# Kernel optimization log

Measured on AMD Instinct MI355X. Metric: run time of the kernel, lower is better.

The kernel has to match this reference:

```python
import jax, jax.numpy as jnp
import numpy as np

B, N, C, H = 2, 2048, 512, 8
D = C // H
SCALE = D ** (-0.5)


def setup_inputs() -> dict:
    key = jax.random.key(0)
    k1, k2, k3 = jax.random.split(key, 3)
    x = jax.random.normal(k1, (B, N, C), dtype=jnp.float32)
    qkv_w = jax.random.normal(k2, (C, 3 * C), dtype=jnp.float32) * (C ** -0.5)
    proj_w = jax.random.normal(k3, (C, C), dtype=jnp.float32) * (C ** -0.5)
    proj_b = jnp.zeros((C,), dtype=jnp.float32)
    return {"x": x, "qkv_w": qkv_w, "proj_w": proj_w, "proj_b": proj_b}


def reference(x, qkv_w, proj_w, proj_b):
    # qkv projection (no bias) -> (B, N, 3, H, D) -> (3, B, H, N, D)
    qkv = jnp.einsum('bnc,cf->bnf', x, qkv_w)
    qkv = qkv.reshape(B, N, 3, H, D).transpose(2, 0, 3, 1, 4)
    q, k, v = qkv[0], qkv[1], qkv[2]
    q = q * SCALE
    attn = jnp.einsum('bhid,bhjd->bhij', q, k)          # (B, H, N, N)
    attn = jax.nn.softmax(attn, axis=-1)
    out = jnp.einsum('bhij,bhjd->bhid', attn, v)         # (B, H, N, D)
    # Faithful to source: reshape (B,H,N,D) -> (B,N,C) WITHOUT transposing
    out = out.reshape(B, N, C)
    out = jnp.einsum('bnc,cd->bnd', out, proj_w) + proj_b
    return out
```

## Files before the change

### kernel.cpp

```cpp
#include <hip/hip_runtime.h>
#include <math.h>

constexpr int Bb = 2;
constexpr int Nn = 2048;
constexpr int Cc = 512;
constexpr int Hh = 8;
constexpr int Dd = 64;

typedef short short8 __attribute__((ext_vector_type(8)));
typedef float floatx4 __attribute__((ext_vector_type(4)));
typedef float floatx16 __attribute__((ext_vector_type(16)));

__device__ inline short8 bcs8(uint4 u) { return __builtin_bit_cast(short8, u); }

__device__ inline floatx4 mfma16(short8 a, short8 b, floatx4 c) {
    return __builtin_amdgcn_mfma_f32_16x16x32_bf16(a, b, c, 0, 0, 0);
}
__device__ inline floatx16 mfma32(short8 a, short8 b, floatx16 c) {
    return __builtin_amdgcn_mfma_f32_32x32x16_bf16(a, b, c, 0, 0, 0);
}

#if __has_builtin(__builtin_amdgcn_exp2f)
#define EXP2(x) __builtin_amdgcn_exp2f(x)
#else
#define EXP2(x) __expf((x) * 0.69314718056f)
#endif

__device__ inline unsigned pk_trunc(float a, float b) {
    return __builtin_amdgcn_perm(__float_as_uint(b), __float_as_uint(a), 0x07060302u);
}
__device__ inline unsigned pk_rne(float a, float b) {
    unsigned ua = __float_as_uint(a); ua += 0x7fffu + ((ua >> 16) & 1u);
    unsigned ub = __float_as_uint(b); ub += 0x7fffu + ((ub >> 16) & 1u);
    return __builtin_amdgcn_perm(ub, ua, 0x07060302u);
}
__device__ inline unsigned short rne1(float a) {
    unsigned u = __float_as_uint(a); u += 0x7fffu + ((u >> 16) & 1u);
    return (unsigned short)(u >> 16);
}
__device__ inline float tr16(float a) {
    return __uint_as_float(__float_as_uint(a) & 0xffff0000u);
}
__device__ inline void split8(float4 A, float4 B, uint4& hi, uint4& lo) {
    hi = make_uint4(pk_trunc(A.x, A.y), pk_trunc(A.z, A.w),
                    pk_trunc(B.x, B.y), pk_trunc(B.z, B.w));
    lo = make_uint4(pk_trunc(A.x - tr16(A.x), A.y - tr16(A.y)),
                    pk_trunc(A.z - tr16(A.z), A.w - tr16(A.w)),
                    pk_trunc(B.x - tr16(B.x), B.y - tr16(B.y)),
                    pk_trunc(B.z - tr16(B.z), B.w - tr16(B.w)));
}


__global__ __launch_bounds__(256) void prep(const float* __restrict__ qkv_w,
                                            const float* __restrict__ proj_w,
                                            const float* __restrict__ x,
                                            unsigned short* __restrict__ wqfrag,
                                            unsigned short* __restrict__ wpfrag,
                                            unsigned short* __restrict__ xfrag)
{
    __shared__ float Tl[64][68];
    int bid = blockIdx.x;
    int t = threadIdx.x;
    if (bid >= 256) {
        int xb = bid - 256;
        int tok = xb * 16 + (t >> 4);
        int kc = t & 15;
        const float* px = x + (size_t)tok * 512 + kc * 32;
        uint4 h[4], l[4];
        #pragma unroll
        for (int o = 0; o < 4; ++o) {
            float4 fa = *(const float4*)(px + o * 8);
            float4 fb = *(const float4*)(px + o * 8 + 4);
            split8(fa, fb, h[o], l[o]);
        }
        int mt = tok >> 4, m = tok & 15;
        unsigned short* fb_ = xfrag + ((size_t)(mt * 16 + kc) * 2) * 512;
        #pragma unroll
        for (int o = 0; o < 4; ++o) {
            *(uint4*)(fb_ + (m + 16 * o) * 8) = h[o];
            *(uint4*)(fb_ + 512 + (m + 16 * o) * 8) = l[o];
        }
        return;
    }
    const float* src; unsigned short* dfrag; int W, f0, k0;
    if (bid < 192) { int kt = bid / 24, ft = bid % 24; W = 1536; src = qkv_w; dfrag = wqfrag; f0 = ft * 64; k0 = kt * 64; }
    else { int b2 = bid - 192; int kt = b2 / 8, ft = b2 % 8; W = 512; src = proj_w; dfrag = wpfrag; f0 = ft * 64; k0 = kt * 64; }
    {
        int kl = t >> 2, fc = (t & 3) * 16;
        const float* p = src + (size_t)(k0 + kl) * W + f0 + fc;
        #pragma unroll
        for (int i = 0; i < 4; ++i) {
            float4 v = *(const float4*)(p + i * 4);
            Tl[kl][fc + i * 4 + 0] = v.x; Tl[kl][fc + i * 4 + 1] = v.y;
            Tl[kl][fc + i * 4 + 2] = v.z; Tl[kl][fc + i * 4 + 3] = v.w;
        }
    }
    __syncthreads();
    {
        int fl = t >> 2, kc16 = (t & 3) * 16;
        float v[16];
        #pragma unroll
        for (int i = 0; i < 16; ++i) v[i] = Tl[kc16 + i][fl];
        unsigned hi[8], lo[8];
        #pragma unroll
        for (int i = 0; i < 8; ++i) {
            float a = v[2 * i], b = v[2 * i + 1];
            hi[i] = pk_trunc(a, b);
            lo[i] = pk_trunc(a - tr16(a), b - tr16(b));
        }
        int f = f0 + fl;
        int nt = f >> 4, nin = f & 15;
        int kc = (k0 + kc16) >> 5;
        int oct0 = (kc16 >> 3) & 3;
        unsigned short* fb_ = dfrag + ((size_t)(nt * 16 + kc) * 2) * 512;
        *(uint4*)(fb_ + (nin + 16 * oct0) * 8) = make_uint4(hi[0], hi[1], hi[2], hi[3]);
        *(uint4*)(fb_ + (nin + 16 * (oct0 + 1)) * 8) = make_uint4(hi[4], hi[5], hi[6], hi[7]);
        *(uint4*)(fb_ + 512 + (nin + 16 * oct0) * 8) = make_uint4(lo[0], lo[1], lo[2], lo[3]);
        *(uint4*)(fb_ + 512 + (nin + 16 * (oct0 + 1)) * 8) = make_uint4(lo[4], lo[5], lo[6], lo[7]);
    }
}

__global__ __launch_bounds__(256, 4) void gemm_qkv(const unsigned short* __restrict__ xfrag,
                                                   const unsigned short* __restrict__ wqfrag,
                                                   unsigned short* __restrict__ qd,
                                                   unsigned short* __restrict__ kfrag,
                                                   unsigned short* __restrict__ vfrag)
{
    const int tid = threadIdx.x, lane = tid & 63, w = tid >> 6;
    const int l15 = lane & 15, l4 = lane >> 4;
    const int row0 = blockIdx.y * 64, col0 = blockIdx.x * 128;
    const int mt0 = row0 >> 4;
    const int nt0 = (col0 >> 4) + w * 2;

    floatx4 acc[4][2];
    #pragma unroll
    for (int i = 0; i < 4; ++i)
        #pragma unroll
        for (int j = 0; j < 2; ++j)
            #pragma unroll
            for (int r = 0; r < 4; ++r) acc[i][j][r] = 0.f;

    const unsigned short* xb = xfrag + (size_t)lane * 8;
    const unsigned short* wb = wqfrag + (size_t)lane * 8;

    #pragma unroll
    for (int kc = 0; kc < 16; ++kc) {
        short8 bf[2][2];
        #pragma unroll
        for (int nt = 0; nt < 2; ++nt) {
            size_t fb_ = ((size_t)((nt0 + nt) * 16 + kc) * 2) * 512;
            bf[nt][0] = bcs8(*(const uint4*)(wb + fb_));
            bf[nt][1] = bcs8(*(const uint4*)(wb + fb_ + 512));
        }
        #pragma unroll
        for (int mt = 0; mt < 4; ++mt) {
            size_t fa_ = ((size_t)((mt0 + mt) * 16 + kc) * 2) * 512;
            short8 ah = bcs8(*(const uint4*)(xb + fa_));
            short8 al = bcs8(*(const uint4*)(xb + fa_ + 512));
            #pragma unroll
            for (int nt = 0; nt < 2; ++nt) {
                acc[mt][nt] = mfma16(ah, bf[nt][0], acc[mt][nt]);
                acc[mt][nt] = mfma16(ah, bf[nt][1], acc[mt][nt]);
                acc[mt][nt] = mfma16(al, bf[nt][0], acc[mt][nt]);
            }
        }
    }
    #pragma unroll
    for (int mt = 0; mt < 4; ++mt)
        #pragma unroll
        for (int nt = 0; nt < 2; ++nt) {
            int c = col0 + (w * 2 + nt) * 16 + l15;
            int which = c >> 9;
            int head = (c >> 6) & 7, d = c & 63;
            int tokb = row0 + mt * 16 + l4 * 4;
            int b = tokb >> 11, n = tokb & 2047;
            int bh = b * 8 + head;
            if (which == 0) {
                #pragma unroll
                for (int r = 0; r < 4; ++r)
                    qd[(size_t)(bh * 2048 + n + r) * 64 + d] = rne1(acc[mt][nt][r] * 0.18033688f);
            } else if (which == 1) {
                int s = d >> 4;
                size_t fb_ = ((size_t)(bh * 64 + (n >> 5)) * 4 + s) * 512 + (d & 7);
                int hl = ((d >> 3) & 1) * 32;
                #pragma unroll
                for (int r = 0; r < 4; ++r)
                    kfrag[fb_ + (size_t)(hl + ((n + r) & 31)) * 8] = rne1(acc[mt][nt][r]);
            } else {
                int j = n >> 4, mtv = d >> 5;
                uint2 pv;
                pv.x = pk_rne(acc[mt][nt][0], acc[mt][nt][1]);
                pv.y = pk_rne(acc[mt][nt][2], acc[mt][nt][3]);
                *(uint2*)&vfrag[((size_t)(bh * 128 + j) * 2 + mtv) * 512 +
                                (size_t)(((n >> 3) & 1) * 32 + (d & 31)) * 8 + (n & 7)] = pv;
            }
        }
}

__global__ __launch_bounds__(256, 4) void attn(const unsigned short* __restrict__ qd,
                                               const unsigned short* __restrict__ kfrag,
                                               const unsigned short* __restrict__ vfrag,
                                               unsigned short* __restrict__ Ofrag)
{
    __shared__ float Ms[2048];
    __shared__ float Ls[64];
    __shared__ float Ts[2176];

    int bid = blockIdx.x;
    int xcd = bid & 7; int rr = bid >> 3;
    int qt = rr & 63; int bhi = rr >> 6;
    int bh = (bhi << 3) | xcd;
    int tid = threadIdx.x, lane = tid & 63, kg = tid >> 6;
    int l31 = lane & 31, h = lane >> 5;

    short8 qf[4];
    #pragma unroll
    for (int s = 0; s < 4; ++s)
        qf[s] = bcs8(*(const uint4*)(qd + ((size_t)bh * 2048 + qt * 32 + l31) * 64 + s * 16 + h * 8));

    const uint4 onesu = make_uint4(0x3F803F80u, 0x3F803F80u, 0x3F803F80u, 0x3F803F80u);
    const short8 onesf = bcs8(onesu);

    floatx16 OT[2], OTl;
    #pragma unroll
    for (int i = 0; i < 2; ++i)
        #pragma unroll
        for (int r = 0; r < 16; ++r) OT[i][r] = 0.f;
    #pragma unroll
    for (int r = 0; r < 16; ++r) OTl[r] = 0.f;

    const unsigned short* kb_ = kfrag + ((size_t)(bh * 64 + kg * 16) * 4) * 512 + lane * 8;
    const unsigned short* vb_ = vfrag + ((size_t)(bh * 128 + kg * 32) * 2) * 512 + lane * 8;

    #pragma unroll
    for (int c = 0; c < 16; ++c) {
        uint4 kfu[4];
        #pragma unroll
        for (int s = 0; s < 4; ++s)
            kfu[s] = *(const uint4*)(kb_ + ((size_t)c * 4 + s) * 512);
        uint4 vfu[2][2];
        #pragma unroll
        for (int kc = 0; kc < 2; ++kc)
            #pragma unroll
            for (int mtv = 0; mtv < 2; ++mtv)
                vfu[kc][mtv] = *(const uint4*)(vb_ + ((size_t)(c * 2 + kc) * 2 + mtv) * 512);

        floatx16 st;
        #pragma unroll
        for (int r = 0; r < 16; ++r) st[r] = 0.f;
        #pragma unroll
        for (int s = 0; s < 4; ++s) st = mfma32(bcs8(kfu[s]), qf[s], st);

        unsigned P2[8];
        #pragma unroll
        for (int s2 = 0; s2 < 8; ++s2)
            P2[s2] = pk_trunc(EXP2(st[2 * s2]), EXP2(st[2 * s2 + 1]));

        #pragma unroll
        for (int kc = 0; kc < 2; ++kc) {
            unsigned X0 = P2[4 * kc + 0], X1 = P2[4 * kc + 1];
            unsigned Y0 = P2[4 * kc + 2], Y1 = P2[4 * kc + 3];
            unsigned T0 = h ? X0 : Y0;
            unsigned T1 = h ? X1 : Y1;
            unsigned To0 = __shfl_xor(T0, 32, 64);
            unsigned To1 = __shfl_xor(T1, 32, 64);
            uint4 fu;
            fu.x = h ? To0 : X0;
            fu.y = h ? To1 : X1;
            fu.z = h ? Y0 : To0;
            fu.w = h ? Y1 : To1;
            short8 pf = bcs8(fu);
            OT[0] = mfma32(bcs8(vfu[kc][0]), pf, OT[0]);
            OT[1] = mfma32(bcs8(vfu[kc][1]), pf, OT[1]);
            OTl = mfma32(onesf, pf, OTl);
        }
    }

    if (kg == 3) {
        #pragma unroll
        for (int mtv = 0; mtv < 2; ++mtv)
            #pragma unroll
            for (int r = 0; r < 16; ++r) {
                int d = mtv * 32 + (r & 3) + 8 * (r >> 2) + 4 * h;
                Ms[d * 32 + l31] = OT[mtv][r];
            }
        Ls[h * 32 + l31] = OTl[0];
    }
    __syncthreads();
    if (kg == 2) {
        #pragma unroll
        for (int mtv = 0; mtv < 2; ++mtv)
            #pragma unroll
            for (int r = 0; r < 16; ++r) {
                int d = mtv * 32 + (r & 3) + 8 * (r >> 2) + 4 * h;
                Ms[d * 32 + l31] += OT[mtv][r];
            }
        Ls[h * 32 + l31] += OTl[0];
    }
    __syncthreads();
    if (kg == 1) {
        #pragma unroll
        for (int mtv = 0; mtv < 2; ++mtv)
            #pragma unroll
            for (int r = 0; r < 16; ++r) {
                int d = mtv * 32 + (r & 3) + 8 * (r >> 2) + 4 * h;
                Ms[d * 32 + l31] += OT[mtv][r];
            }
        Ls[h * 32 + l31] += OTl[0];
    }
    __syncthreads();
    if (kg == 0) {
        #pragma unroll
        for (int mtv = 0; mtv < 2; ++mtv)
            #pragma unroll
            for (int r = 0; r < 16; ++r) {
                int d = mtv * 32 + (r & 3) + 8 * (r >> 2) + 4 * h;
                OT[mtv][r] += Ms[d * 32 + l31];
            }
        float inv = 1.f / (Ls[h * 32 + l31] + OTl[0]);
        #pragma unroll
        for (int mtv = 0; mtv < 2; ++mtv)
            #pragma unroll
            for (int r = 0; r < 16; ++r) {
                int d = mtv * 32 + (r & 3) + 8 * (r >> 2) + 4 * h;
                Ts[l31 * 68 + d] = OT[mtv][r] * inv;
            }
    }
    __syncthreads();
    {
        int q = tid >> 3, dc = (tid & 7) * 8;
        float vv[8];
        #pragma unroll
        for (int i = 0; i < 8; ++i) vv[i] = Ts[q * 68 + dc + i];
        unsigned hi[4], lo[4];
        #pragma unroll
        for (int i = 0; i < 4; ++i) {
            float a = vv[2 * i], bb = vv[2 * i + 1];
            hi[i] = pk_trunc(a, bb);
            lo[i] = pk_trunc(a - tr16(a), bb - tr16(bb));
        }
        int ng = qt * 32 + q;
        int r = bh * 256 + (ng >> 3);
        int cc = (ng & 7) * 64 + dc;
        int mt = r >> 4, m = r & 15, kc = cc >> 5, oct = (cc >> 3) & 3;
        unsigned short* fb_ = Ofrag + ((size_t)(mt * 16 + kc) * 2) * 512 + (m + 16 * oct) * 8;
        *(uint4*)fb_ = make_uint4(hi[0], hi[1], hi[2], hi[3]);
        *(uint4*)(fb_ + 512) = make_uint4(lo[0], lo[1], lo[2], lo[3]);
    }
}

__global__ __launch_bounds__(256, 4) void gemm_proj(const unsigned short* __restrict__ Ofrag,
                                                    const unsigned short* __restrict__ wpfrag,
                                                    const float* __restrict__ bias,
                                                    float* __restrict__ out)
{
    const int tid = threadIdx.x, lane = tid & 63, w = tid >> 6;
    const int l15 = lane & 15, l4 = lane >> 4;
    const int row0 = blockIdx.y * 64, col0 = blockIdx.x * 64;
    const int wm = w >> 1, wn = w & 1;
    const int mt0 = (row0 >> 4) + wm * 2;
    const int nt0 = (col0 >> 4) + wn * 2;

    floatx4 acc[2][2];
    #pragma unroll
    for (int i = 0; i < 2; ++i)
        #pragma unroll
        for (int j = 0; j < 2; ++j)
            #pragma unroll
            for (int r = 0; r < 4; ++r) acc[i][j][r] = 0.f;

    const unsigned short* ab = Ofrag + (size_t)lane * 8;
    const unsigned short* wb = wpfrag + (size_t)lane * 8;

    #pragma unroll
    for (int kc = 0; kc < 16; ++kc) {
        short8 bf[2][2];
        #pragma unroll
        for (int nt = 0; nt < 2; ++nt) {
            size_t fb_ = ((size_t)((nt0 + nt) * 16 + kc) * 2) * 512;
            bf[nt][0] = bcs8(*(const uint4*)(wb + fb_));
            bf[nt][1] = bcs8(*(const uint4*)(wb + fb_ + 512));
        }
        #pragma unroll
        for (int mt = 0; mt < 2; ++mt) {
            size_t fa_ = ((size_t)((mt0 + mt) * 16 + kc) * 2) * 512;
            short8 ah = bcs8(*(const uint4*)(ab + fa_));
            short8 al = bcs8(*(const uint4*)(ab + fa_ + 512));
            #pragma unroll
            for (int nt = 0; nt < 2; ++nt) {
                acc[mt][nt] = mfma16(ah, bf[nt][0], acc[mt][nt]);
                acc[mt][nt] = mfma16(ah, bf[nt][1], acc[mt][nt]);
                acc[mt][nt] = mfma16(al, bf[nt][0], acc[mt][nt]);
            }
        }
    }
    #pragma unroll
    for (int mt = 0; mt < 2; ++mt)
        #pragma unroll
        for (int nt = 0; nt < 2; ++nt) {
            int c = col0 + wn * 32 + nt * 16 + l15;
            float bv = bias[c];
            #pragma unroll
            for (int r = 0; r < 4; ++r) {
                int tok = row0 + wm * 32 + mt * 16 + l4 * 4 + r;
                out[(size_t)tok * 512 + c] = acc[mt][nt][r] + bv;
            }
        }
}

extern "C" void kernel_launch(void* const* d_in, const int* in_sizes, int n_in,
                              void* d_out, int out_size, void* d_ws, size_t ws_size,
                              hipStream_t stream)
{
    const float* x      = (const float*)d_in[0];
    const float* qkv_w  = (const float*)d_in[1];
    const float* proj_w = (const float*)d_in[2];
    const float* proj_b = (const float*)d_in[3];
    float* out = (float*)d_out;

    char* ws = (char*)d_ws;
    unsigned short* xfrag  = (unsigned short*)ws;
    unsigned short* wqfrag = (unsigned short*)(ws + 8388608);
    unsigned short* wpfrag = (unsigned short*)(ws + 11534336);
    unsigned short* qd     = (unsigned short*)(ws + 12582912);
    unsigned short* kfrag  = (unsigned short*)(ws + 16777216);
    unsigned short* vfrag  = (unsigned short*)(ws + 20971520);
    unsigned short* Ofrag  = (unsigned short*)(ws + 25165824);

    prep<<<512, 256, 0, stream>>>(qkv_w, proj_w, x, wqfrag, wpfrag, xfrag);
    gemm_qkv<<<dim3(12, 64), 256, 0, stream>>>(xfrag, wqfrag, qd, kfrag, vfrag);
    attn<<<1024, 256, 0, stream>>>(qd, kfrag, vfrag, Ofrag);
    gemm_proj<<<dim3(8, 64), 256, 0, stream>>>(Ofrag, wpfrag, proj_b, out);
}
```

Measured before the change: 140.4 us.

## Process two query tiles per attention block to reuse K/V fragments

```diff
diff --git a/kernel.cpp b/kernel.cpp
--- a/kernel.cpp
+++ b/kernel.cpp
@@ -120,7 +120,7 @@
     }
 }
 
-__global__ __launch_bounds__(256, 4) void gemm_qkv(const unsigned short* __restrict__ xfrag,
+__global__ __launch_bounds__(256, 3) void gemm_qkv(const unsigned short* __restrict__ xfrag,
                                                    const unsigned short* __restrict__ wqfrag,
                                                    unsigned short* __restrict__ qd,
                                                    unsigned short* __restrict__ kfrag,
@@ -197,37 +197,42 @@
         }
 }
 
-__global__ __launch_bounds__(256, 4) void attn(const unsigned short* __restrict__ qd,
+__global__ __launch_bounds__(256, 2) void attn(const unsigned short* __restrict__ qd,
                                                const unsigned short* __restrict__ kfrag,
                                                const unsigned short* __restrict__ vfrag,
                                                unsigned short* __restrict__ Ofrag)
 {
-    __shared__ float Ms[2048];
-    __shared__ float Ls[64];
-    __shared__ float Ts[2176];
+    __shared__ float Ms[4096];
+    __shared__ float Ls[128];
+    __shared__ float Ts[64 * 68];
 
     int bid = blockIdx.x;
     int xcd = bid & 7; int rr = bid >> 3;
-    int qt = rr & 63; int bhi = rr >> 6;
+    int qt = rr & 31; int bhi = rr >> 5;
     int bh = (bhi << 3) | xcd;
     int tid = threadIdx.x, lane = tid & 63, kg = tid >> 6;
     int l31 = lane & 31, h = lane >> 5;
 
-    short8 qf[4];
-    #pragma unroll
-    for (int s = 0; s < 4; ++s)
-        qf[s] = bcs8(*(const uint4*)(qd + ((size_t)bh * 2048 + qt * 32 + l31) * 64 + s * 16 + h * 8));
+    short8 qf[2][4];
+    #pragma unroll
+    for (int qh = 0; qh < 2; ++qh)
+        #pragma unroll
+        for (int s = 0; s < 4; ++s)
+            qf[qh][s] = bcs8(*(const uint4*)(qd + ((size_t)bh * 2048 + qt * 64 + qh * 32 + l31) * 64 + s * 16 + h * 8));
 
     const uint4 onesu = make_uint4(0x3F803F80u, 0x3F803F80u, 0x3F803F80u, 0x3F803F80u);
     const short8 onesf = bcs8(onesu);
 
-    floatx16 OT[2], OTl;
-    #pragma unroll
-    for (int i = 0; i < 2; ++i)
-        #pragma unroll
-        for (int r = 0; r < 16; ++r) OT[i][r] = 0.f;
-    #pragma unroll
-    for (int r = 0; r < 16; ++r) OTl[r] = 0.f;
+    floatx16 OT[2][2], OTl[2];
+    #pragma unroll
+    for (int qh = 0; qh < 2; ++qh) {
+        #pragma unroll
+        for (int i = 0; i < 2; ++i)
+            #pragma unroll
+            for (int r = 0; r < 16; ++r) OT[qh][i][r] = 0.f;
+        #pragma unroll
+        for (int r = 0; r < 16; ++r) OTl[qh][r] = 0.f;
+    }
 
     const unsigned short* kb_ = kfrag + ((size_t)(bh * 64 + kg * 16) * 4) * 512 + lane * 8;
     const unsigned short* vb_ = vfrag + ((size_t)(bh * 128 + kg * 32) * 2) * 512 + lane * 8;
@@ -245,111 +250,130 @@
             for (int mtv = 0; mtv < 2; ++mtv)
                 vfu[kc][mtv] = *(const uint4*)(vb_ + ((size_t)(c * 2 + kc) * 2 + mtv) * 512);
 
-        floatx16 st;
-        #pragma unroll
-        for (int r = 0; r < 16; ++r) st[r] = 0.f;
-        #pragma unroll
-        for (int s = 0; s < 4; ++s) st = mfma32(bcs8(kfu[s]), qf[s], st);
-
-        unsigned P2[8];
-        #pragma unroll
-        for (int s2 = 0; s2 < 8; ++s2)
-            P2[s2] = pk_trunc(EXP2(st[2 * s2]), EXP2(st[2 * s2 + 1]));
-
-        #pragma unroll
-        for (int kc = 0; kc < 2; ++kc) {
-            unsigned X0 = P2[4 * kc + 0], X1 = P2[4 * kc + 1];
-            unsigned Y0 = P2[4 * kc + 2], Y1 = P2[4 * kc + 3];
-            unsigned T0 = h ? X0 : Y0;
-            unsigned T1 = h ? X1 : Y1;
-            unsigned To0 = __shfl_xor(T0, 32, 64);
-            unsigned To1 = __shfl_xor(T1, 32, 64);
-            uint4 fu;
-            fu.x = h ? To0 : X0;
-            fu.y = h ? To1 : X1;
-            fu.z = h ? Y0 : To0;
-            fu.w = h ? Y1 : To1;
-            short8 pf = bcs8(fu);
-            OT[0] = mfma32(bcs8(vfu[kc][0]), pf, OT[0]);
-            OT[1] = mfma32(bcs8(vfu[kc][1]), pf, OT[1]);
-            OTl = mfma32(onesf, pf, OTl);
+        #pragma unroll
+        for (int qh = 0; qh < 2; ++qh) {
+            floatx16 st;
+            #pragma unroll
+            for (int r = 0; r < 16; ++r) st[r] = 0.f;
+            #pragma unroll
+            for (int s = 0; s < 4; ++s) st = mfma32(bcs8(kfu[s]), qf[qh][s], st);
+
+            unsigned P2[8];
+            #pragma unroll
+            for (int s2 = 0; s2 < 8; ++s2)
+                P2[s2] = pk_trunc(EXP2(st[2 * s2]), EXP2(st[2 * s2 + 1]));
+
+            #pragma unroll
+            for (int kc = 0; kc < 2; ++kc) {
+                unsigned X0 = P2[4 * kc + 0], X1 = P2[4 * kc + 1];
+                unsigned Y0 = P2[4 * kc + 2], Y1 = P2[4 * kc + 3];
+                unsigned T0 = h ? X0 : Y0;
+                unsigned T1 = h ? X1 : Y1;
+                unsigned To0 = __shfl_xor(T0, 32, 64);
+                unsigned To1 = __shfl_xor(T1, 32, 64);
+                uint4 fu;
+                fu.x = h ? To0 : X0;
+                fu.y = h ? To1 : X1;
+                fu.z = h ? Y0 : To0;
+                fu.w = h ? Y1 : To1;
+                short8 pf = bcs8(fu);
+                OT[qh][0] = mfma32(bcs8(vfu[kc][0]), pf, OT[qh][0]);
+                OT[qh][1] = mfma32(bcs8(vfu[kc][1]), pf, OT[qh][1]);
+                OTl[qh] = mfma32(onesf, pf, OTl[qh]);
+            }
         }
     }
 
     if (kg == 3) {
         #pragma unroll
-        for (int mtv = 0; mtv < 2; ++mtv)
-            #pragma unroll
-            for (int r = 0; r < 16; ++r) {
-                int d = mtv * 32 + (r & 3) + 8 * (r >> 2) + 4 * h;
-                Ms[d * 32 + l31] = OT[mtv][r];
-            }
-        Ls[h * 32 + l31] = OTl[0];
+        for (int qh = 0; qh < 2; ++qh) {
+            #pragma unroll
+            for (int mtv = 0; mtv < 2; ++mtv)
+                #pragma unroll
+                for (int r = 0; r < 16; ++r) {
+                    int d = mtv * 32 + (r & 3) + 8 * (r >> 2) + 4 * h;
+                    Ms[d * 64 + qh * 32 + l31] = OT[qh][mtv][r];
+                }
+            Ls[h * 64 + qh * 32 + l31] = OTl[qh][0];
+        }
     }
     __syncthreads();
     if (kg == 2) {
         #pragma unroll
-        for (int mtv = 0; mtv < 2; ++mtv)
-            #pragma unroll
-            for (int r = 0; r < 16; ++r) {
-                int d = mtv * 32 + (r & 3) + 8 * (r >> 2) + 4 * h;
-                Ms[d * 32 + l31] += OT[mtv][r];
-            }
-        Ls[h * 32 + l31] += OTl[0];
+        for (int qh = 0; qh < 2; ++qh) {
+            #pragma unroll
+            for (int mtv = 0; mtv < 2; ++mtv)
+                #pragma unroll
+                for (int r = 0; r < 16; ++r) {
+                    int d = mtv * 32 + (r & 3) + 8 * (r >> 2) + 4 * h;
+                    Ms[d * 64 + qh * 32 + l31] += OT[qh][mtv][r];
+                }
+            Ls[h * 64 + qh * 32 + l31] += OTl[qh][0];
+        }
     }
     __syncthreads();
     if (kg == 1) {
         #pragma unroll
-        for (int mtv = 0; mtv < 2; ++mtv)
-            #pragma unroll
-            for (int r = 0; r < 16; ++r) {
-                int d = mtv * 32 + (r & 3) + 8 * (r >> 2) + 4 * h;
-                Ms[d * 32 + l31] += OT[mtv][r];
-            }
-        Ls[h * 32 + l31] += OTl[0];
+        for (int qh = 0; qh < 2; ++qh) {
+            #pragma unroll
+            for (int mtv = 0; mtv < 2; ++mtv)
+                #pragma unroll
+                for (int r = 0; r < 16; ++r) {
+                    int d = mtv * 32 + (r & 3) + 8 * (r >> 2) + 4 * h;
+                    Ms[d * 64 + qh * 32 + l31] += OT[qh][mtv][r];
+                }
+            Ls[h * 64 + qh * 32 + l31] += OTl[qh][0];
+        }
     }
     __syncthreads();
     if (kg == 0) {
         #pragma unroll
-        for (int mtv = 0; mtv < 2; ++mtv)
-            #pragma unroll
-            for (int r = 0; r < 16; ++r) {
-                int d = mtv * 32 + (r & 3) + 8 * (r >> 2) + 4 * h;
-                OT[mtv][r] += Ms[d * 32 + l31];
-            }
-        float inv = 1.f / (Ls[h * 32 + l31] + OTl[0]);
-        #pragma unroll
-        for (int mtv = 0; mtv < 2; ++mtv)
-            #pragma unroll
-            for (int r = 0; r < 16; ++r) {
-                int d = mtv * 32 + (r & 3) + 8 * (r >> 2) + 4 * h;
-                Ts[l31 * 68 + d] = OT[mtv][r] * inv;
-            }
+        for (int qh = 0; qh < 2; ++qh) {
+            #pragma unroll
+            for (int mtv = 0; mtv < 2; ++mtv)
+                #pragma unroll
+                for (int r = 0; r < 16; ++r) {
+                    int d = mtv * 32 + (r & 3) + 8 * (r >> 2) + 4 * h;
+                    OT[qh][mtv][r] += Ms[d * 64 + qh * 32 + l31];
+                }
+            float inv = 1.f / (Ls[h * 64 + qh * 32 + l31] + OTl[qh][0]);
+            #pragma unroll
+            for (int mtv = 0; mtv < 2; ++mtv)
+                #pragma unroll
+                for (int r = 0; r < 16; ++r) {
+                    int d = mtv * 32 + (r & 3) + 8 * (r >> 2) + 4 * h;
+                    Ts[(qh * 32 + l31) * 68 + d] = OT[qh][mtv][r] * inv;
+                }
+        }
     }
     __syncthreads();
     {
-        int q = tid >> 3, dc = (tid & 7) * 8;
-        float vv[8];
-        #pragma unroll
-        for (int i = 0; i < 8; ++i) vv[i] = Ts[q * 68 + dc + i];
-        unsigned hi[4], lo[4];
-        #pragma unroll
-        for (int i = 0; i < 4; ++i) {
+        int q = tid >> 2, dc = (tid & 3) * 16;
+        float vv[16];
+        #pragma unroll
+        for (int i = 0; i < 16; ++i) vv[i] = Ts[q * 68 + dc + i];
+        unsigned hi[8], lo[8];
+        #pragma unroll
+        for (int i = 0; i < 8; ++i) {
             float a = vv[2 * i], bb = vv[2 * i + 1];
             hi[i] = pk_trunc(a, bb);
             lo[i] = pk_trunc(a - tr16(a), bb - tr16(bb));
         }
-        int ng = qt * 32 + q;
+        int ng = qt * 64 + q;
         int r = bh * 256 + (ng >> 3);
-        int cc = (ng & 7) * 64 + dc;
-        int mt = r >> 4, m = r & 15, kc = cc >> 5, oct = (cc >> 3) & 3;
-        unsigned short* fb_ = Ofrag + ((size_t)(mt * 16 + kc) * 2) * 512 + (m + 16 * oct) * 8;
-        *(uint4*)fb_ = make_uint4(hi[0], hi[1], hi[2], hi[3]);
-        *(uint4*)(fb_ + 512) = make_uint4(lo[0], lo[1], lo[2], lo[3]);
-    }
-}
-
-__global__ __launch_bounds__(256, 4) void gemm_proj(const unsigned short* __restrict__ Ofrag,
+        int mt = r >> 4, m = r & 15;
+        #pragma unroll
+        for (int hh = 0; hh < 2; ++hh) {
+            int cc = (ng & 7) * 64 + dc + hh * 8;
+            int kc = cc >> 5, oct = (cc >> 3) & 3;
+            unsigned short* fb_ = Ofrag + ((size_t)(mt * 16 + kc) * 2) * 512 + (m + 16 * oct) * 8;
+            *(uint4*)fb_ = make_uint4(hi[4 * hh + 0], hi[4 * hh + 1], hi[4 * hh + 2], hi[4 * hh + 3]);
+            *(uint4*)(fb_ + 512) = make_uint4(lo[4 * hh + 0], lo[4 * hh + 1], lo[4 * hh + 2], lo[4 * hh + 3]);
+        }
+    }
+}
+
+__global__ __launch_bounds__(256, 2) void gemm_proj(const unsigned short* __restrict__ Ofrag,
                                                     const unsigned short* __restrict__ wpfrag,
                                                     const float* __restrict__ bias,
                                                     float* __restrict__ out)
@@ -429,6 +453,6 @@
 
     prep<<<512, 256, 0, stream>>>(qkv_w, proj_w, x, wqfrag, wpfrag, xfrag);
     gemm_qkv<<<dim3(12, 64), 256, 0, stream>>>(xfrag, wqfrag, qd, kfrag, vfrag);
-    attn<<<1024, 256, 0, stream>>>(qd, kfrag, vfrag, Ofrag);
+    attn<<<512, 256, 0, stream>>>(qd, kfrag, vfrag, Ofrag);
     gemm_proj<<<dim3(8, 64), 256, 0, stream>>>(Ofrag, wpfrag, proj_b, out);
 }
```

Result: faster. 136.2 us (-3.0%).
